# Kernel optimization log

Measured on AMD Instinct MI355X. Metric: run time of the kernel, lower is better.

## Reference

```python
import math
import jax, jax.numpy as jnp
import numpy as np
from jax import lax

B, C, O, K, WDIM, H, W = 8, 512, 512, 3, 512, 64, 64
CONV_SCALE = 1.0 / math.sqrt(C * K * K)
MOD_SCALE = 1.0 / math.sqrt(WDIM)


def setup_inputs() -> dict:
    key = jax.random.key(0)
    k1, k2, k3, k4 = jax.random.split(key, 4)
    return {
        "x": jax.random.normal(k1, (B, C, H, W), dtype=jnp.float32),
        "w": jax.random.normal(k2, (B, WDIM), dtype=jnp.float32),
        "base_weight": jax.random.normal(k3, (1, O, C, K, K), dtype=jnp.float32),
        "mod_weight": jax.random.normal(k4, (C, WDIM), dtype=jnp.float32),
        "mod_bias": jnp.zeros((C,), dtype=jnp.float32),
    }


def reference(x, w, base_weight, mod_weight, mod_bias):
    # EqualLinear modulation: s in (B, C), then +1
    s = w @ (mod_weight * MOD_SCALE).T + mod_bias + 1.0  # (B, C)
    # Per-sample modulated weights: (B, O, C, K, K)
    weight = CONV_SCALE * base_weight * s[:, None, :, None, None]
    # Demodulation
    d = lax.rsqrt(jnp.sum(weight * weight, axis=(2, 3, 4), keepdims=True))
    weight = weight * d
    pad = K // 2

    def conv_one(xi, wi):
        # xi: (C, H, W), wi: (O, C, K, K)
        return lax.conv_general_dilated(
            xi[None], wi, window_strides=(1, 1),
            padding=[(pad, pad), (pad, pad)],
            dimension_numbers=("NCHW", "OIHW", "NCHW"),
        )[0]

    return jax.vmap(conv_one)(x, weight)  # (B, O, H, W)
```

## Files before the change

### kernel.cpp

```cpp
#include <hip/hip_runtime.h>
#include <stdint.h>


#define MOD_SCALE  0.044194173824159216f
#define CONV_SCALE 0.014731391274719739f

typedef __attribute__((ext_vector_type(4))) float f32x4;
typedef __attribute__((ext_vector_type(8))) short bf16x8;

__device__ inline unsigned short f2bf(float f) {
  uint32_t u = __float_as_uint(f);
  uint32_t r = (u + 0x7fffu + ((u >> 16) & 1u)) >> 16;
  return (unsigned short)r;
}

__device__ inline void gload_lds16(const void* g, void* l) {
  __builtin_amdgcn_global_load_lds(
      (const __attribute__((address_space(1))) void*)g,
      (__attribute__((address_space(3))) void*)l, 16, 0, 0);
}

__global__ __launch_bounds__(256) void k_style(const float* __restrict__ w,
                                               const float* __restrict__ modw,
                                               const float* __restrict__ modb,
                                               float* __restrict__ s_out) {
  __shared__ float red[256];
  const int tid = threadIdx.x;
  const int sb = blockIdx.x;
  const int cb = sb & 7, b = sb >> 3;
  const int cl = tid >> 2, qq = tid & 3;
  const int c = (cb << 6) + cl;
  const float4* wd = (const float4*)(w + (b << 9) + (qq << 7));
  const float4* md = (const float4*)(modw + ((size_t)c << 9) + (qq << 7));
  float acc = 0.f;
#pragma unroll
  for (int i = 0; i < 32; ++i) {
    float4 a = wd[i], m = md[i];
    acc += a.x * m.x + a.y * m.y + a.z * m.z + a.w * m.w;
  }
  red[tid] = acc;
  __syncthreads();
  if (tid < 64) {
    float v = red[tid * 4] + red[tid * 4 + 1] + red[tid * 4 + 2] + red[tid * 4 + 3];
    int cc = (cb << 6) + tid;
    s_out[(b << 9) + cc] = v * MOD_SCALE + modb[cc] + 1.0f;
  }
}

__global__ __launch_bounds__(256) void k_mid(const float* __restrict__ bw,
                                             const float* __restrict__ s,
                                             unsigned short* __restrict__ awT,
                                             float* __restrict__ d_out,
                                             const float* __restrict__ x,
                                             unsigned short* __restrict__ xp) {
  __shared__ uint32_t tb[64 * 260];
  const int blk = blockIdx.x;
  const int tid = threadIdx.x;

  if (blk < 512) {
    float* lw  = (float*)tb;
    float* ls  = lw + 4608;
    float* red = ls + 4096;
    const int o = blk;
    {
      const float4* src = (const float4*)(bw + (size_t)o * 4608);
      float4* dst = (float4*)lw;
#pragma unroll
      for (int i = 0; i < 4; ++i) dst[tid + (i << 8)] = src[tid + (i << 8)];
      if (tid < 128) dst[tid + 1024] = src[tid + 1024];
    }
    {
      const float4* src = (const float4*)s;
      float4* dst = (float4*)ls;
#pragma unroll
      for (int i = 0; i < 4; ++i) dst[tid + (i << 8)] = src[tid + (i << 8)];
    }
    __syncthreads();
    const int c0 = tid << 1;
    const int base = c0 * 9;
    float wq0 = 0.f, wq1 = 0.f;
#pragma unroll
    for (int j = 0; j < 9; ++j) {
      float a = lw[base + j];      wq0 += a * a;
      float b2 = lw[base + 9 + j]; wq1 += b2 * b2;
    }
    const int lane = tid & 63, wv = tid >> 6;
#pragma unroll
    for (int b = 0; b < 8; ++b) {
      float s0 = ls[(b << 9) + c0], s1 = ls[(b << 9) + c0 + 1];
      float v = wq0 * s0 * s0 + wq1 * s1 * s1;
#pragma unroll
      for (int off = 32; off > 0; off >>= 1) v += __shfl_down(v, off, 64);
      if (lane == 0) red[(b << 2) + wv] = v;
    }
    __syncthreads();
    if (tid < 8) {
      float a = red[tid << 2] + red[(tid << 2) + 1] + red[(tid << 2) + 2] + red[(tid << 2) + 3];
      d_out[(tid << 9) + o] = rsqrtf(a * (1.0f / 4608.0f)) * CONV_SCALE;
    }
    uint32_t* dst = (uint32_t*)(awT + (size_t)o * 4608);
#pragma unroll
    for (int j = 0; j < 9; ++j)
      dst[(j << 8) + tid] = (uint32_t)f2bf(lw[base + j]) |
                            ((uint32_t)f2bf(lw[base + 9 + j]) << 16);
  } else if (blk < 1024) {
    const int q = blk - 512;
    const int b = q >> 6, y = q & 63;
    const int px4 = tid & 15;
    const int cp  = tid >> 4;
    const float* xb = x + (size_t)(b << 9) * 4096 + (y << 6) + (px4 << 2);
    const float* sb = s + (b << 9);
#pragma unroll
    for (int it = 0; it < 16; ++it) {
      const int cpair = cp + (it << 4);
      const int c0 = cpair << 1;
      const float4 a0 = *(const float4*)(xb + (size_t)c0 * 4096);
      const float4 a1 = *(const float4*)(xb + (size_t)(c0 + 1) * 4096);
      const float s0 = sb[c0], s1 = sb[c0 + 1];
      const int pxb = px4 << 2;
      tb[(pxb + 0) * 260 + cpair] = (uint32_t)f2bf(a0.x * s0) | ((uint32_t)f2bf(a1.x * s1) << 16);
      tb[(pxb + 1) * 260 + cpair] = (uint32_t)f2bf(a0.y * s0) | ((uint32_t)f2bf(a1.y * s1) << 16);
      tb[(pxb + 2) * 260 + cpair] = (uint32_t)f2bf(a0.z * s0) | ((uint32_t)f2bf(a1.z * s1) << 16);
      tb[(pxb + 3) * 260 + cpair] = (uint32_t)f2bf(a0.w * s0) | ((uint32_t)f2bf(a1.w * s1) << 16);
    }
    __syncthreads();
    const int wv = tid >> 6, l = tid & 63;
    uint32_t* xpw = (uint32_t*)xp;
#pragma unroll
    for (int it = 0; it < 16; ++it) {
      const int px = (wv << 4) + it;
      const uint4 v = *(const uint4*)(tb + px * 260 + (l << 2));
      const size_t base = ((size_t)b * 4356 + (size_t)(y + 1) * 66 + (px + 1)) << 8;
      ((uint4*)(xpw + base))[l] = v;
    }
  } else {
    const int q = blk - 1024;
    const int b = q / 260, p = q - b * 260;
    int py, px;
    if (p < 66)       { py = 0;       px = p; }
    else if (p < 132) { py = 65;      px = p - 66; }
    else if (p < 196) { py = p - 131; px = 0; }
    else              { py = p - 195; px = 65; }
    uint32_t* dst = (uint32_t*)(xp + ((size_t)b * 4356 + py * 66 + px) * 512);
    dst[tid] = 0u;
  }
}

__global__ __launch_bounds__(256, 2) void k_conv(const unsigned short* __restrict__ awT,
                                                 const unsigned short* __restrict__ xpad,
                                                 const float* __restrict__ dmod,
                                                 float* __restrict__ out) {
  __shared__ alignas(16) unsigned short As[3 * 8192];
  __shared__ alignas(16) unsigned short Bs[8448];
  const int tid = threadIdx.x;
  const int b  = blockIdx.z;
  const int m0 = blockIdx.y << 7;
  const int n0 = blockIdx.x << 7;
  const int y0 = n0 >> 6;

  const int srow = tid >> 3;
  const int schk = ((tid & 7) - (srow & 7)) & 7;
  const int scol = schk << 3;

  const unsigned short* A0 = awT + (size_t)(m0 + srow) * 4608 + scol;
  const size_t bx = (size_t)b * (66 * 66 * 512);

  const int lane = tid & 63;
  const int wv   = tid >> 6;
  const int moff = (wv >> 1) << 6;
  const int noff = (wv & 1) << 6;
  const int noffp = noff ? 66 : 0;
  const int lm   = lane & 15;
  const int g4   = lane >> 4;

  const unsigned short* ardA[2];
#pragma unroll
  for (int h = 0; h < 2; ++h)
    ardA[h] = As + (moff + lm) * 64 + ((((h << 2) + g4) + moff + lm) & 7) * 8;
  const unsigned short* ardB[3][2];
#pragma unroll
  for (int kx = 0; kx < 3; ++kx) {
    const int rb = noffp + lm + kx;
#pragma unroll
    for (int h = 0; h < 2; ++h)
      ardB[kx][h] = Bs + rb * 64 + ((((h << 2) + g4) + rb) & 7) * 8;
  }

  f32x4 acc[4][4];
#pragma unroll
  for (int i = 0; i < 4; ++i)
#pragma unroll
    for (int j = 0; j < 4; ++j) acc[i][j] = (f32x4){0.f, 0.f, 0.f, 0.f};

#pragma unroll 1
  for (int ky = 0; ky < 3; ++ky) {
    const unsigned short* Bp0 = xpad + bx + (size_t)((y0 + ky) * 66 + srow) * 512 + scol;
#pragma unroll 1
    for (int kb = 0; kb < 8; ++kb) {
      const int kcol = kb << 6;
#pragma unroll
      for (int kx = 0; kx < 3; ++kx) {
        const unsigned short* Ap = A0 + ((ky * 3 + kx) << 9) + kcol;
#pragma unroll
        for (int g = 0; g < 4; ++g)
          gload_lds16(Ap + g * (32 * 4608), As + ((kx << 13) + (((g << 8) + tid) << 3)));
      }
      const unsigned short* Bp = Bp0 + kcol;
#pragma unroll
      for (int g = 0; g < 4; ++g)
        gload_lds16(Bp + g * (32 * 512), Bs + (((g << 8) + tid) << 3));
      if (tid < 32) gload_lds16(Bp + 128 * 512, Bs + 8192 + tid * 8);
      __syncthreads();
#pragma unroll
      for (int kx = 0; kx < 3; ++kx) {
#pragma unroll
        for (int h = 0; h < 2; ++h) {
          bf16x8 af[4], bf[4];
          const unsigned short* pa = ardA[h] + (kx << 13);
          const unsigned short* pb = ardB[kx][h];
#pragma unroll
          for (int i = 0; i < 4; ++i) af[i] = *(const bf16x8*)(pa + (i << 10));
#pragma unroll
          for (int j = 0; j < 4; ++j) bf[j] = *(const bf16x8*)(pb + (j << 10));
#pragma unroll
          for (int i = 0; i < 4; ++i)
#pragma unroll
            for (int j = 0; j < 4; ++j)
              acc[i][j] = __builtin_amdgcn_mfma_f32_16x16x32_bf16(af[i], bf[j], acc[i][j], 0, 0, 0);
        }
      }
      __syncthreads();
    }
  }

  const float* dB = dmod + (b << 9) + m0 + moff;
  float* op = out + (size_t)((b << 9) + m0 + moff) * 4096 + n0 + noff;
#pragma unroll
  for (int i = 0; i < 4; ++i) {
#pragma unroll
    for (int r = 0; r < 4; ++r) {
      const int m = i * 16 + (g4 << 2) + r;
      const float dm = dB[m];
#pragma unroll
      for (int j = 0; j < 4; ++j)
        op[(size_t)m * 4096 + (j << 4) + lm] = acc[i][j][r] * dm;
    }
  }
}

extern "C" void kernel_launch(void* const* d_in, const int* in_sizes, int n_in,
                              void* d_out, int out_size, void* d_ws, size_t ws_size,
                              hipStream_t stream) {
  const float* x    = (const float*)d_in[0];
  const float* w    = (const float*)d_in[1];
  const float* bw   = (const float*)d_in[2];
  const float* modw = (const float*)d_in[3];
  const float* modb = (const float*)d_in[4];
  float* out = (float*)d_out;
  char* ws = (char*)d_ws;

  float* s_buf = (float*)(ws);
  float* d_buf = (float*)(ws + 16384);
  unsigned short* awT  = (unsigned short*)(ws + 32768);
  unsigned short* xpad = (unsigned short*)(ws + 4751360);

  (void)in_sizes; (void)n_in; (void)out_size; (void)ws_size;

  k_style<<<64,   256, 0, stream>>>(w, modw, modb, s_buf);
  k_mid  <<<3104, 256, 0, stream>>>(bw, s_buf, awT, d_buf, x, xpad);
  k_conv <<<dim3(32, 4, 8), 256, 0, stream>>>(awT, xpad, d_buf, out);
}
```

Baseline: 266.3 us.

## Enlarge conv tiles to 256x256 with double-buffered LDS prefetch pipeline

The implicit-GEMM conv kernel moves from 128x128 tiles with 256 threads to 256x256 tiles with 512 threads. Shared A and B buffers become double-buffered so the next kx/kb slice is loaded while MFMAs run on the current one, and MFMA sections raise wave priority. The aim is to hide global-to-LDS latency and raise operand reuse per byte loaded. The cost is larger LDS use and 128 accumulator registers per lane, which limits occupancy to one block per CU and leaves only 256 blocks in the grid.

```diff
diff --git a/kernel.cpp b/kernel.cpp
--- a/kernel.cpp
+++ b/kernel.cpp
@@ -146,17 +146,19 @@
   }
 }
 
-__global__ __launch_bounds__(256, 2) void k_conv(const unsigned short* __restrict__ awT,
+__global__ __launch_bounds__(512, 1) void k_conv(const unsigned short* __restrict__ awT,
                                                  const unsigned short* __restrict__ xpad,
                                                  const float* __restrict__ dmod,
                                                  float* __restrict__ out) {
-  __shared__ alignas(16) unsigned short As[3 * 8192];
-  __shared__ alignas(16) unsigned short Bs[8448];
+  __shared__ alignas(16) unsigned short As[2][16384];
+  __shared__ alignas(16) unsigned short Bs[2][16896];
   const int tid = threadIdx.x;
+
+  const int nI = blockIdx.x;
+  const int m0 = blockIdx.y << 8;
   const int b  = blockIdx.z;
-  const int m0 = blockIdx.y << 7;
-  const int n0 = blockIdx.x << 7;
-  const int y0 = n0 >> 6;
+  const int n0 = nI << 8;
+  const int y0 = nI << 2;
 
   const int srow = tid >> 3;
   const int schk = ((tid & 7) - (srow & 7)) & 7;
@@ -164,77 +166,101 @@
 
   const unsigned short* A0 = awT + (size_t)(m0 + srow) * 4608 + scol;
   const size_t bx = (size_t)b * (66 * 66 * 512);
+  const unsigned short* B0 = xpad + bx + (size_t)(y0 * 66 + srow) * 512 + scol;
 
   const int lane = tid & 63;
   const int wv   = tid >> 6;
   const int moff = (wv >> 1) << 6;
-  const int noff = (wv & 1) << 6;
-  const int noffp = noff ? 66 : 0;
   const int lm   = lane & 15;
   const int g4   = lane >> 4;
 
-  const unsigned short* ardA[2];
+  const int arow = moff + lm;
+  int aoff[2];
 #pragma unroll
   for (int h = 0; h < 2; ++h)
-    ardA[h] = As + (moff + lm) * 64 + ((((h << 2) + g4) + moff + lm) & 7) * 8;
-  const unsigned short* ardB[3][2];
-#pragma unroll
-  for (int kx = 0; kx < 3; ++kx) {
-    const int rb = noffp + lm + kx;
-#pragma unroll
-    for (int h = 0; h < 2; ++h)
-      ardB[kx][h] = Bs + rb * 64 + ((((h << 2) + g4) + rb) & 7) * 8;
-  }
-
-  f32x4 acc[4][4];
+    aoff[h] = arow * 64 + ((((h << 2) + g4) + arow) & 7) * 8;
+  int boff[3][2][2];
+#pragma unroll
+  for (int kx = 0; kx < 3; ++kx)
+#pragma unroll
+    for (int jr = 0; jr < 2; ++jr) {
+      const int rb = ((wv & 1) * 2 + jr) * 66 + lm + kx;
+#pragma unroll
+      for (int h = 0; h < 2; ++h)
+        boff[kx][jr][h] = rb * 64 + ((((h << 2) + g4) + rb) & 7) * 8;
+    }
+
+  f32x4 acc[4][8];
 #pragma unroll
   for (int i = 0; i < 4; ++i)
 #pragma unroll
-    for (int j = 0; j < 4; ++j) acc[i][j] = (f32x4){0.f, 0.f, 0.f, 0.f};
-
+    for (int j = 0; j < 8; ++j) acc[i][j] = (f32x4){0.f, 0.f, 0.f, 0.f};
+
+  auto stageA = [&](int buf, int ky, int kx, int kb) {
+    const unsigned short* Ap = A0 + (((ky * 3 + kx) << 9) + (kb << 6));
+#pragma unroll
+    for (int g = 0; g < 4; ++g)
+      gload_lds16(Ap + (size_t)(g << 6) * 4608, &As[buf][(g << 12) + (tid << 3)]);
+  };
+  auto stageB = [&](int buf, int ky, int kb) {
+    const unsigned short* Bp = B0 + (size_t)(ky * 66) * 512 + (kb << 6);
+#pragma unroll
+    for (int g = 0; g < 4; ++g)
+      gload_lds16(Bp + (size_t)(g << 6) * 512, &Bs[buf][(g << 12) + (tid << 3)]);
+    if (tid < 64) gload_lds16(Bp + (size_t)256 * 512, &Bs[buf][16384 + (tid << 3)]);
+  };
+  auto mstep = [&](int ab, int bb, int kx) {
+    __builtin_amdgcn_s_setprio(1);
+#pragma unroll
+    for (int h = 0; h < 2; ++h) {
+      bf16x8 af[4], bfr[8];
+      const unsigned short* pa = As[ab] + aoff[h];
+#pragma unroll
+      for (int i = 0; i < 4; ++i) af[i] = *(const bf16x8*)(pa + (i << 10));
+#pragma unroll
+      for (int j = 0; j < 8; ++j)
+        bfr[j] = *(const bf16x8*)(Bs[bb] + boff[kx][j >> 2][h] + ((j & 3) << 10));
+#pragma unroll
+      for (int i = 0; i < 4; ++i)
+#pragma unroll
+        for (int j = 0; j < 8; ++j)
+          acc[i][j] = __builtin_amdgcn_mfma_f32_16x16x32_bf16(af[i], bfr[j], acc[i][j], 0, 0, 0);
+    }
+    __builtin_amdgcn_s_setprio(0);
+  };
+
+  stageA(0, 0, 0, 0);
+  stageB(0, 0, 0);
+  __syncthreads();
+
+  int ab = 0, bb = 0;
 #pragma unroll 1
   for (int ky = 0; ky < 3; ++ky) {
-    const unsigned short* Bp0 = xpad + bx + (size_t)((y0 + ky) * 66 + srow) * 512 + scol;
 #pragma unroll 1
     for (int kb = 0; kb < 8; ++kb) {
-      const int kcol = kb << 6;
-#pragma unroll
-      for (int kx = 0; kx < 3; ++kx) {
-        const unsigned short* Ap = A0 + ((ky * 3 + kx) << 9) + kcol;
-#pragma unroll
-        for (int g = 0; g < 4; ++g)
-          gload_lds16(Ap + g * (32 * 4608), As + ((kx << 13) + (((g << 8) + tid) << 3)));
+      stageA(ab ^ 1, ky, 1, kb);
+      mstep(ab, bb, 0);
+      __syncthreads();
+      ab ^= 1;
+      stageA(ab ^ 1, ky, 2, kb);
+      mstep(ab, bb, 1);
+      __syncthreads();
+      ab ^= 1;
+      const int nky = (kb == 7) ? ky + 1 : ky;
+      const int nkb = (kb == 7) ? 0 : kb + 1;
+      if (!(ky == 2 && kb == 7)) {
+        stageA(ab ^ 1, nky, 0, nkb);
+        stageB(bb ^ 1, nky, nkb);
       }
-      const unsigned short* Bp = Bp0 + kcol;
-#pragma unroll
-      for (int g = 0; g < 4; ++g)
-        gload_lds16(Bp + g * (32 * 512), Bs + (((g << 8) + tid) << 3));
-      if (tid < 32) gload_lds16(Bp + 128 * 512, Bs + 8192 + tid * 8);
+      mstep(ab, bb, 2);
       __syncthreads();
-#pragma unroll
-      for (int kx = 0; kx < 3; ++kx) {
-#pragma unroll
-        for (int h = 0; h < 2; ++h) {
-          bf16x8 af[4], bf[4];
-          const unsigned short* pa = ardA[h] + (kx << 13);
-          const unsigned short* pb = ardB[kx][h];
-#pragma unroll
-          for (int i = 0; i < 4; ++i) af[i] = *(const bf16x8*)(pa + (i << 10));
-#pragma unroll
-          for (int j = 0; j < 4; ++j) bf[j] = *(const bf16x8*)(pb + (j << 10));
-#pragma unroll
-          for (int i = 0; i < 4; ++i)
-#pragma unroll
-            for (int j = 0; j < 4; ++j)
-              acc[i][j] = __builtin_amdgcn_mfma_f32_16x16x32_bf16(af[i], bf[j], acc[i][j], 0, 0, 0);
-        }
-      }
-      __syncthreads();
+      ab ^= 1;
+      bb ^= 1;
     }
   }
 
   const float* dB = dmod + (b << 9) + m0 + moff;
-  float* op = out + (size_t)((b << 9) + m0 + moff) * 4096 + n0 + noff;
+  float* op = out + (size_t)((b << 9) + m0 + moff) * 4096 + n0 + ((wv & 1) << 7);
 #pragma unroll
   for (int i = 0; i < 4; ++i) {
 #pragma unroll
@@ -242,7 +268,7 @@
       const int m = i * 16 + (g4 << 2) + r;
       const float dm = dB[m];
 #pragma unroll
-      for (int j = 0; j < 4; ++j)
+      for (int j = 0; j < 8; ++j)
         op[(size_t)m * 4096 + (j << 4) + lm] = acc[i][j][r] * dm;
     }
   }
@@ -268,5 +294,5 @@
 
   k_style<<<64,   256, 0, stream>>>(w, modw, modb, s_buf);
   k_mid  <<<3104, 256, 0, stream>>>(bw, s_buf, awT, d_buf, x, xpad);
-  k_conv <<<dim3(32, 4, 8), 256, 0, stream>>>(awT, xpad, d_buf, out);
-}
+  k_conv <<<dim3(16, 2, 8), 512, 0, stream>>>(awT, xpad, d_buf, out);
+}
```

Result: no change. 265.1 us (-0.5%).
